# Performance work log

Hardware: AMD Instinct MI355X
Metric: run time of the kernel (lower is better)

The kernel has to match this reference:

```python
import jax, jax.numpy as jnp
import numpy as np

D_MODEL = 1024
HIDDEN = 64
N_STEPS = 6
T0, T1 = 0.0, 1.0


def setup_inputs() -> dict:
    key = jax.random.key(0)
    kx, k1, k2, k3, k4 = jax.random.split(key, 5)
    # PyTorch nn.Linear default init: U(-1/sqrt(fan_in), 1/sqrt(fan_in))
    s1 = 1.0 / np.sqrt(D_MODEL + 1)
    s2 = 1.0 / np.sqrt(HIDDEN)
    return {
        "x": jax.random.normal(kx, (8, 2048, D_MODEL), dtype=jnp.float32),
        "W1": jax.random.uniform(k1, (D_MODEL + 1, HIDDEN), jnp.float32, -s1, s1),
        "b1": jax.random.uniform(k2, (HIDDEN,), jnp.float32, -s1, s1),
        "W2": jax.random.uniform(k3, (HIDDEN, D_MODEL), jnp.float32, -s2, s2),
        "b2": jax.random.uniform(k4, (D_MODEL,), jnp.float32, -s2, s2),
    }


def _dynamics(t, z, W1, b1, W2, b2):
    # Equivalent to concat([z, t*ones], -1) @ W1: split the last row of W1
    # (the time channel) so we avoid materializing the concat.
    h = jnp.tanh(jnp.einsum("btd,dh->bth", z, W1[:-1]) + t * W1[-1] + b1)
    return jnp.einsum("bth,hd->btd", h, W2) + b2


def reference(x, W1, b1, W2, b2):
    h = (T1 - T0) / N_STEPS  # step size
    ts = T0 + h * jnp.arange(N_STEPS, dtype=x.dtype)

    def rk4_step(z, t):
        k1 = _dynamics(t, z, W1, b1, W2, b2)
        k2 = _dynamics(t + h / 2, z + (h / 2) * k1, W1, b1, W2, b2)
        k3 = _dynamics(t + h / 2, z + (h / 2) * k2, W1, b1, W2, b2)
        k4 = _dynamics(t + h, z + h * k3, W1, b1, W2, b2)
        z_next = z + (h / 6) * (k1 + 2 * k2 + 2 * k3 + k4)
        return z_next, None

    z_T, _ = jax.lax.scan(rk4_step, x, ts)
    return z_T
```

## Files before the change

### kernel.cpp

```cpp
#include <hip/hip_runtime.h>
#include <hip/hip_bf16.h>

#define DM 1024
#define HID 64
#define NSTEP 6
#define RSTEP (1.0f/6.0f)

using short8  = __attribute__((ext_vector_type(8))) short;
using short4v = __attribute__((ext_vector_type(4))) short;
using f32x4   = __attribute__((ext_vector_type(4))) float;

#define WS_W1P 0
#define WS_W2P 131072
#define WS_GP  262144
#define WS_U   270336
#define WS_VST 270592
#define WS_HU  276736

#define L_H   0
#define L_VST 2304
#define L_HU  8448
#define L_B2  8704
#define LDS_TOTAL 12800
#define HP 144

#define FENCE() asm volatile("s_waitcnt lgkmcnt(0)" ::: "memory")

__device__ __forceinline__ short f2bf(float f) {
    __hip_bfloat16 h = __float2bfloat16(f);
    short s;
    __builtin_memcpy(&s, &h, 2);
    return s;
}
__device__ __forceinline__ float ftanh(float x) {
    x = fminf(fmaxf(x, -10.f), 10.f);
    float e = __expf(2.f * x);
    return __fdividef(e - 1.f, e + 1.f);
}

__global__ void k_prep(const float* __restrict__ W1, const float* __restrict__ W2,
                       const float* __restrict__ b1, const float* __restrict__ b2,
                       short* __restrict__ W1P, short* __restrict__ W2P,
                       short* __restrict__ GP, float* __restrict__ U,
                       float* __restrict__ VST, float* __restrict__ HU) {
    __shared__ float red[4][64];
    int b = blockIdx.x;
    int t = threadIdx.x;
    int l = t & 63, q4 = t >> 6;
    if (b < 32) {
        int kk = b, c = q4;
        int col = c * 16 + (l & 15);
        int kb = kk * 32 + ((l >> 4) << 3);
        short8 v;
        #pragma unroll
        for (int i = 0; i < 8; ++i) v[i] = f2bf(W1[(kb + i) * HID + col]);
        *(short8*)(W1P + (((kk * 4 + c) * 64) + l) * 8) = v;
    } else if (b < 64) {
        int unit = (b - 32) * 4 + q4;
        int kk2 = unit >> 6, ct = unit & 63;
        int col = ct * 16 + (l & 15);
        int kb = kk2 * 32 + ((l >> 4) << 3);
        short8 v;
        #pragma unroll
        for (int i = 0; i < 8; ++i) v[i] = f2bf(W2[(kb + i) * DM + col]);
        *(short8*)(W2P + (((kk2 * 64 + ct) * 64) + l) * 8) = v;
    } else if (b < 128) {
        int j = b - 64;
        float acc = 0.f;
        #pragma unroll 8
        for (int d = q4 * 256; d < q4 * 256 + 256; ++d)
            acc += W2[j * DM + d] * W1[d * HID + l];
        red[q4][l] = acc;
        __syncthreads();
        if (t < 64) {
            float a = red[0][l] + red[1][l] + red[2][l] + red[3][l];
            int kk = j >> 5, lk = (j >> 3) & 3, ii = j & 7, c = l >> 4, lo = l & 15;
            GP[(((kk * 4 + c) * 64) + lk * 16 + lo) * 8 + ii] = f2bf(a);
        }
    } else {
        float acc = 0.f;
        #pragma unroll 8
        for (int d = q4 * 256; d < q4 * 256 + 256; ++d)
            acc += b2[d] * W1[d * HID + l];
        red[q4][l] = acc;
        __syncthreads();
        if (t < 64) {
            float uu = red[0][l] + red[1][l] + red[2][l] + red[3][l];
            U[l] = uu;
            HU[l] = RSTEP * uu;
            float b1l = b1[l];
            float wtl = W1[DM * HID + l];
            #pragma unroll
            for (int s6 = 0; s6 < 6; ++s6) {
                float ts = RSTEP * (float)s6;
                float tm = ts + 0.5f * RSTEP;
                float vmid = b1l + tm * wtl + 0.5f * RSTEP * uu;
                VST[(s6 * 4 + 0) * 64 + l] = b1l + ts * wtl;
                VST[(s6 * 4 + 1) * 64 + l] = vmid;
                VST[(s6 * 4 + 2) * 64 + l] = vmid;
                VST[(s6 * 4 + 3) * 64 + l] = b1l + (ts + RSTEP) * wtl + RSTEP * uu;
            }
        }
    }
}

#define EPL(W0,W1,W2,W3,X0,X1,P) \
    W0 = w2p8[(P) * 64 + lane];        W1 = w2p8[((P) + 64) * 64 + lane]; \
    W2 = w2p8[((P) + 1) * 64 + lane];  W3 = w2p8[((P) + 65) * 64 + lane]; \
    X0 = *(const f32x4*)(xrow + (P) * 16 + (hq << 2)); \
    X1 = *(const f32x4*)(xrow + ((P) + 1) * 16 + (hq << 2));

#define EPC(W0,W1,W2,W3,X0,X1,P) { \
    f32x4 p0 = (f32x4){0.f,0.f,0.f,0.f}, p1 = (f32x4){0.f,0.f,0.f,0.f}; \
    p0 = __builtin_amdgcn_mfma_f32_16x16x32_bf16(W0, sb0, p0, 0, 0, 0); \
    p0 = __builtin_amdgcn_mfma_f32_16x16x32_bf16(W1, sb1, p0, 0, 0, 0); \
    p1 = __builtin_amdgcn_mfma_f32_16x16x32_bf16(W2, sb0, p1, 0, 0, 0); \
    p1 = __builtin_amdgcn_mfma_f32_16x16x32_bf16(W3, sb1, p1, 0, 0, 0); \
    f32x4 b0v = *(const f32x4*)(smem + L_B2 + ((P) * 16 + (hq << 2)) * 4); \
    f32x4 b1v = *(const f32x4*)(smem + L_B2 + (((P) + 1) * 16 + (hq << 2)) * 4); \
    f32x4 n0, n1; \
    for (int j = 0; j < 4; ++j) { n0[j] = X0[j] + p0[j] + b0v[j]; \
                                  n1[j] = X1[j] + p1[j] + b1v[j]; } \
    *(f32x4*)(orow + (P) * 16 + (hq << 2)) = n0; \
    *(f32x4*)(orow + ((P) + 1) * 16 + (hq << 2)) = n1; }

__global__ __launch_bounds__(64) __attribute__((amdgpu_waves_per_eu(2, 4)))
void k_ode(
        const float* __restrict__ X, const float* __restrict__ b2,
        const short* __restrict__ W1P, const short* __restrict__ W2P,
        const short* __restrict__ GP, const float* __restrict__ VST,
        const float* __restrict__ HU, float* __restrict__ OUT) {
    extern __shared__ char smem[];
    const int lane = threadIdx.x & 63;
    const int hq = lane >> 4;
    const int l15 = lane & 15;
    const size_t row0 = (size_t)blockIdx.x * 16;
    const float* xrow = X + (row0 + l15) * DM;

    #pragma unroll
    for (int i = 0; i < 4; ++i)
        *(f32x4*)(smem + L_B2 + lane * 64 + i * 16) =
            *(const f32x4*)(b2 + lane * 16 + i * 4);

    f32x4 sz[4] = {(f32x4){0.f,0.f,0.f,0.f}, (f32x4){0.f,0.f,0.f,0.f},
                   (f32x4){0.f,0.f,0.f,0.f}, (f32x4){0.f,0.f,0.f,0.f}};
    {
        const short8* wp = (const short8*)W1P;
        #pragma unroll
        for (int B = 0; B < 4; ++B) {
            f32x4 lo[8], hi[8];
            #pragma unroll
            for (int i = 0; i < 8; ++i) {
                const float* xp = xrow + ((B * 8 + i) << 5) + (hq << 3);
                lo[i] = *(const f32x4*)(xp);
                hi[i] = *(const f32x4*)(xp + 4);
            }
            #pragma unroll
            for (int i = 0; i < 8; ++i) {
                int kk = B * 8 + i;
                short8 zf;
                #pragma unroll
                for (int j = 0; j < 4; ++j) { zf[j] = f2bf(lo[i][j]); zf[4 + j] = f2bf(hi[i][j]); }
                #pragma unroll
                for (int c = 0; c < 4; ++c)
                    sz[c] = __builtin_amdgcn_mfma_f32_16x16x32_bf16(
                                wp[(kk * 4 + c) * 64 + lane], zf, sz[c], 0, 0, 0);
            }
        }
    }

    #pragma unroll
    for (int i = 0; i < 6; ++i)
        *(f32x4*)(smem + L_VST + i * 1024 + lane * 16) =
            *(const f32x4*)(VST + i * 256 + lane * 4);
    if (lane < 16)
        *(f32x4*)(smem + L_HU + lane * 16) = *(const f32x4*)(HU + lane * 4);
    short8 gfr[2][4];
    #pragma unroll
    for (int k2 = 0; k2 < 2; ++k2)
        #pragma unroll
        for (int c = 0; c < 4; ++c)
            gfr[k2][c] = *(const short8*)(GP + ((k2 * 4 + c) * 64 + lane) * 8);
    FENCE();

    f32x4 ssum[4] = {(f32x4){0.f,0.f,0.f,0.f}, (f32x4){0.f,0.f,0.f,0.f},
                     (f32x4){0.f,0.f,0.f,0.f}, (f32x4){0.f,0.f,0.f,0.f}};

    for (int s = 0; s < NSTEP; ++s) {
        f32x4 hsum[4];

        #pragma unroll
        for (int c = 0; c < 4; ++c) {
            f32x4 vst = *(const f32x4*)(smem + L_VST + (s * 4 + 0) * 256 + c * 64 + (hq << 4));
            short4v hc;
            #pragma unroll
            for (int j = 0; j < 4; ++j) {
                float h = ftanh(sz[c][j] + vst[j]);
                hsum[c][j] = h;
                hc[j] = f2bf(h);
            }
            *(short4v*)(smem + L_H + l15 * HP + c * 32 + (hq << 3)) = hc;
        }
        FENCE();

        #pragma unroll
        for (int e = 1; e < 4; ++e) {
            const float ce = (e == 3) ? RSTEP : (0.5f * RSTEP);
            const float we = (e == 3) ? 1.f : 2.f;
            short8 hf0 = *(const short8*)(smem + L_H + l15 * HP + (hq << 4));
            short8 hf1 = *(const short8*)(smem + L_H + l15 * HP + 64 + (hq << 4));
            #pragma unroll
            for (int c = 0; c < 4; ++c) {
                f32x4 dd = (f32x4){0.f, 0.f, 0.f, 0.f};
                dd = __builtin_amdgcn_mfma_f32_16x16x32_bf16(gfr[0][c], hf0, dd, 0, 0, 0);
                dd = __builtin_amdgcn_mfma_f32_16x16x32_bf16(gfr[1][c], hf1, dd, 0, 0, 0);
                f32x4 vst = *(const f32x4*)(smem + L_VST + (s * 4 + e) * 256 + c * 64 + (hq << 4));
                short4v hc;
                #pragma unroll
                for (int j = 0; j < 4; ++j) {
                    float h = ftanh(sz[c][j] + ce * dd[j] + vst[j]);
                    hsum[c][j] += we * h;
                    if (e < 3) {
                        hc[j] = f2bf(h);
                    } else {
                        ssum[c][j] += hsum[c][j] * (RSTEP / 6.f);
                        hc[j] = (s < NSTEP - 1) ? f2bf(hsum[c][j] * (RSTEP / 6.f))
                                                : f2bf(ssum[c][j]);
                    }
                }
                *(short4v*)(smem + L_H + l15 * HP + c * 32 + (hq << 3)) = hc;
            }
            FENCE();
        }

        if (s < NSTEP - 1) {
            short8 hb0 = *(const short8*)(smem + L_H + l15 * HP + (hq << 4));
            short8 hb1 = *(const short8*)(smem + L_H + l15 * HP + 64 + (hq << 4));
            #pragma unroll
            for (int c = 0; c < 4; ++c) {
                f32x4 d = (f32x4){0.f, 0.f, 0.f, 0.f};
                d = __builtin_amdgcn_mfma_f32_16x16x32_bf16(gfr[0][c], hb0, d, 0, 0, 0);
                d = __builtin_amdgcn_mfma_f32_16x16x32_bf16(gfr[1][c], hb1, d, 0, 0, 0);
                f32x4 hu4 = *(const f32x4*)(smem + L_HU + c * 64 + (hq << 4));
                #pragma unroll
                for (int j = 0; j < 4; ++j)
                    sz[c][j] += d[j] + hu4[j];
            }
        }
    }

    {
        short8 sb0 = *(const short8*)(smem + L_H + l15 * HP + (hq << 4));
        short8 sb1 = *(const short8*)(smem + L_H + l15 * HP + 64 + (hq << 4));
        const short8* w2p8 = (const short8*)W2P;
        float* orow = OUT + (row0 + l15) * DM;

        short8 wA0, wA1, wA2, wA3; f32x4 xA0, xA1;
        short8 wB0, wB1, wB2, wB3; f32x4 xB0, xB1;
        EPL(wA0, wA1, wA2, wA3, xA0, xA1, 0)
        #pragma unroll
        for (int p = 0; p < 64; p += 4) {
            EPL(wB0, wB1, wB2, wB3, xB0, xB1, p + 2)
            EPC(wA0, wA1, wA2, wA3, xA0, xA1, p)
            if (p + 4 < 64) { EPL(wA0, wA1, wA2, wA3, xA0, xA1, p + 4) }
            EPC(wB0, wB1, wB2, wB3, xB0, xB1, p + 2)
        }
    }
}

extern "C" void kernel_launch(void* const* d_in, const int* in_sizes, int n_in,
                              void* d_out, int out_size, void* d_ws, size_t ws_size,
                              hipStream_t stream) {
    (void)in_sizes; (void)n_in; (void)out_size; (void)ws_size;
    const float* X  = (const float*)d_in[0];
    const float* W1 = (const float*)d_in[1];
    const float* b1 = (const float*)d_in[2];
    const float* W2 = (const float*)d_in[3];
    const float* b2 = (const float*)d_in[4];
    float* OUT = (float*)d_out;
    short* W1P = (short*)((char*)d_ws + WS_W1P);
    short* W2P = (short*)((char*)d_ws + WS_W2P);
    short* GP  = (short*)((char*)d_ws + WS_GP);
    float* U   = (float*)((char*)d_ws + WS_U);
    float* VST = (float*)((char*)d_ws + WS_VST);
    float* HU  = (float*)((char*)d_ws + WS_HU);

    k_prep<<<129, 256, 0, stream>>>(W1, W2, b1, b2, W1P, W2P, GP, U, VST, HU);
    k_ode<<<1024, 64, LDS_TOTAL, stream>>>(X, b2, W1P, W2P, GP, VST, HU, OUT);
}
```

Measured before the change: 72.14 us.

## Split hidden dimension across four waves per block with barrier-synchronized LDS exchange

```diff
diff --git a/kernel.cpp b/kernel.cpp
--- a/kernel.cpp
+++ b/kernel.cpp
@@ -17,14 +17,16 @@
 #define WS_VST 270592
 #define WS_HU  276736
 
-#define L_H   0
-#define L_VST 2304
-#define L_HU  8448
-#define L_B2  8704
-#define LDS_TOTAL 12800
+#define L_H0  0
+#define L_H1  2304
+#define L_HB  4608
+#define L_VST 6912
+#define L_HU  13056
+#define L_B2  13312
+#define LDS_TOTAL 17408
 #define HP 144
 
-#define FENCE() asm volatile("s_waitcnt lgkmcnt(0)" ::: "memory")
+#define BAR() asm volatile("s_waitcnt lgkmcnt(0)\n\ts_barrier" ::: "memory")
 
 __device__ __forceinline__ short f2bf(float f) {
     __hip_bfloat16 h = __float2bfloat16(f);
@@ -104,46 +106,53 @@
     }
 }
 
-#define EPL(W0,W1,W2,W3,X0,X1,P) \
-    W0 = w2p8[(P) * 64 + lane];        W1 = w2p8[((P) + 64) * 64 + lane]; \
-    W2 = w2p8[((P) + 1) * 64 + lane];  W3 = w2p8[((P) + 65) * 64 + lane]; \
-    X0 = *(const f32x4*)(xrow + (P) * 16 + (hq << 2)); \
-    X1 = *(const f32x4*)(xrow + ((P) + 1) * 16 + (hq << 2));
-
-#define EPC(W0,W1,W2,W3,X0,X1,P) { \
-    f32x4 p0 = (f32x4){0.f,0.f,0.f,0.f}, p1 = (f32x4){0.f,0.f,0.f,0.f}; \
-    p0 = __builtin_amdgcn_mfma_f32_16x16x32_bf16(W0, sb0, p0, 0, 0, 0); \
-    p0 = __builtin_amdgcn_mfma_f32_16x16x32_bf16(W1, sb1, p0, 0, 0, 0); \
-    p1 = __builtin_amdgcn_mfma_f32_16x16x32_bf16(W2, sb0, p1, 0, 0, 0); \
-    p1 = __builtin_amdgcn_mfma_f32_16x16x32_bf16(W3, sb1, p1, 0, 0, 0); \
-    f32x4 b0v = *(const f32x4*)(smem + L_B2 + ((P) * 16 + (hq << 2)) * 4); \
-    f32x4 b1v = *(const f32x4*)(smem + L_B2 + (((P) + 1) * 16 + (hq << 2)) * 4); \
-    f32x4 n0, n1; \
-    for (int j = 0; j < 4; ++j) { n0[j] = X0[j] + p0[j] + b0v[j]; \
-                                  n1[j] = X1[j] + p1[j] + b1v[j]; } \
-    *(f32x4*)(orow + (P) * 16 + (hq << 2)) = n0; \
-    *(f32x4*)(orow + ((P) + 1) * 16 + (hq << 2)) = n1; }
-
-__global__ __launch_bounds__(64) __attribute__((amdgpu_waves_per_eu(2, 4)))
+#define EPL(Wa,Wb,Wc,Wd,Xa,Xb,P) \
+    Wa = w2p8[(P) * 64 + lane];        Wb = w2p8[((P) + 64) * 64 + lane]; \
+    Wc = w2p8[((P) + 1) * 64 + lane];  Wd = w2p8[((P) + 65) * 64 + lane]; \
+    Xa = *(const f32x4*)(xrow + (P) * 16 + (hq << 2)); \
+    Xb = *(const f32x4*)(xrow + ((P) + 1) * 16 + (hq << 2));
+
+#define EPC(Wa,Wb,Wc,Wd,Xa,Xb,P) { \
+    f32x4 acc0 = (f32x4){0.f,0.f,0.f,0.f}, acc1 = (f32x4){0.f,0.f,0.f,0.f}; \
+    acc0 = __builtin_amdgcn_mfma_f32_16x16x32_bf16(Wa, sb0, acc0, 0, 0, 0); \
+    acc0 = __builtin_amdgcn_mfma_f32_16x16x32_bf16(Wb, sb1, acc0, 0, 0, 0); \
+    acc1 = __builtin_amdgcn_mfma_f32_16x16x32_bf16(Wc, sb0, acc1, 0, 0, 0); \
+    acc1 = __builtin_amdgcn_mfma_f32_16x16x32_bf16(Wd, sb1, acc1, 0, 0, 0); \
+    f32x4 epc_bv0 = *(const f32x4*)(smem + L_B2 + ((P) * 16 + (hq << 2)) * 4); \
+    f32x4 epc_bv1 = *(const f32x4*)(smem + L_B2 + (((P) + 1) * 16 + (hq << 2)) * 4); \
+    f32x4 epc_n0, epc_n1; \
+    for (int j = 0; j < 4; ++j) { epc_n0[j] = Xa[j] + acc0[j] + epc_bv0[j]; \
+                                  epc_n1[j] = Xb[j] + acc1[j] + epc_bv1[j]; } \
+    *(f32x4*)(orow + (P) * 16 + (hq << 2)) = epc_n0; \
+    *(f32x4*)(orow + ((P) + 1) * 16 + (hq << 2)) = epc_n1; }
+
+__global__ __launch_bounds__(256) __attribute__((amdgpu_waves_per_eu(2, 4)))
 void k_ode(
         const float* __restrict__ X, const float* __restrict__ b2,
         const short* __restrict__ W1P, const short* __restrict__ W2P,
         const short* __restrict__ GP, const float* __restrict__ VST,
         const float* __restrict__ HU, float* __restrict__ OUT) {
     extern __shared__ char smem[];
-    const int lane = threadIdx.x & 63;
+    const int t = threadIdx.x;
+    const int lane = t & 63;
+    const int w = t >> 6;
     const int hq = lane >> 4;
     const int l15 = lane & 15;
+    const int hcol0 = w * 16 + hq * 4;
     const size_t row0 = (size_t)blockIdx.x * 16;
     const float* xrow = X + (row0 + l15) * DM;
 
-    #pragma unroll
-    for (int i = 0; i < 4; ++i)
-        *(f32x4*)(smem + L_B2 + lane * 64 + i * 16) =
-            *(const f32x4*)(b2 + lane * 16 + i * 4);
-
-    f32x4 sz[4] = {(f32x4){0.f,0.f,0.f,0.f}, (f32x4){0.f,0.f,0.f,0.f},
-                   (f32x4){0.f,0.f,0.f,0.f}, (f32x4){0.f,0.f,0.f,0.f}};
+    *(f32x4*)(smem + L_B2 + t * 16) = *(const f32x4*)(b2 + t * 4);
+    *(f32x4*)(smem + L_VST + t * 16) = *(const f32x4*)(VST + t * 4);
+    if (t < 128)
+        *(f32x4*)(smem + L_VST + 4096 + t * 16) = *(const f32x4*)(VST + 1024 + t * 4);
+    else if (t < 144)
+        *(f32x4*)(smem + L_HU + (t - 128) * 16) = *(const f32x4*)(HU + (t - 128) * 4);
+
+    short8 gf0 = *(const short8*)(GP + (w * 64 + lane) * 8);
+    short8 gf1 = *(const short8*)(GP + ((4 + w) * 64 + lane) * 8);
+
+    f32x4 sz = (f32x4){0.f, 0.f, 0.f, 0.f};
     {
         const short8* wp = (const short8*)W1P;
         #pragma unroll
@@ -161,109 +170,90 @@
                 short8 zf;
                 #pragma unroll
                 for (int j = 0; j < 4; ++j) { zf[j] = f2bf(lo[i][j]); zf[4 + j] = f2bf(hi[i][j]); }
-                #pragma unroll
-                for (int c = 0; c < 4; ++c)
-                    sz[c] = __builtin_amdgcn_mfma_f32_16x16x32_bf16(
-                                wp[(kk * 4 + c) * 64 + lane], zf, sz[c], 0, 0, 0);
-            }
-        }
-    }
-
-    #pragma unroll
-    for (int i = 0; i < 6; ++i)
-        *(f32x4*)(smem + L_VST + i * 1024 + lane * 16) =
-            *(const f32x4*)(VST + i * 256 + lane * 4);
-    if (lane < 16)
-        *(f32x4*)(smem + L_HU + lane * 16) = *(const f32x4*)(HU + lane * 4);
-    short8 gfr[2][4];
-    #pragma unroll
-    for (int k2 = 0; k2 < 2; ++k2)
-        #pragma unroll
-        for (int c = 0; c < 4; ++c)
-            gfr[k2][c] = *(const short8*)(GP + ((k2 * 4 + c) * 64 + lane) * 8);
-    FENCE();
-
-    f32x4 ssum[4] = {(f32x4){0.f,0.f,0.f,0.f}, (f32x4){0.f,0.f,0.f,0.f},
-                     (f32x4){0.f,0.f,0.f,0.f}, (f32x4){0.f,0.f,0.f,0.f}};
+                sz = __builtin_amdgcn_mfma_f32_16x16x32_bf16(
+                         wp[(kk * 4 + w) * 64 + lane], zf, sz, 0, 0, 0);
+            }
+        }
+    }
+    BAR();
+
+    f32x4 ssum = (f32x4){0.f, 0.f, 0.f, 0.f};
 
     for (int s = 0; s < NSTEP; ++s) {
-        f32x4 hsum[4];
-
-        #pragma unroll
-        for (int c = 0; c < 4; ++c) {
-            f32x4 vst = *(const f32x4*)(smem + L_VST + (s * 4 + 0) * 256 + c * 64 + (hq << 4));
+        f32x4 hsum;
+
+        {
+            f32x4 vst = *(const f32x4*)(smem + L_VST + (s * 4 + 0) * 256 + hcol0 * 4);
             short4v hc;
             #pragma unroll
             for (int j = 0; j < 4; ++j) {
-                float h = ftanh(sz[c][j] + vst[j]);
-                hsum[c][j] = h;
+                float h = ftanh(sz[j] + vst[j]);
+                hsum[j] = h;
                 hc[j] = f2bf(h);
             }
-            *(short4v*)(smem + L_H + l15 * HP + c * 32 + (hq << 3)) = hc;
-        }
-        FENCE();
+            *(short4v*)(smem + L_H0 + l15 * HP + hcol0 * 2) = hc;
+        }
+        BAR();
 
         #pragma unroll
         for (int e = 1; e < 4; ++e) {
             const float ce = (e == 3) ? RSTEP : (0.5f * RSTEP);
             const float we = (e == 3) ? 1.f : 2.f;
-            short8 hf0 = *(const short8*)(smem + L_H + l15 * HP + (hq << 4));
-            short8 hf1 = *(const short8*)(smem + L_H + l15 * HP + 64 + (hq << 4));
-            #pragma unroll
-            for (int c = 0; c < 4; ++c) {
-                f32x4 dd = (f32x4){0.f, 0.f, 0.f, 0.f};
-                dd = __builtin_amdgcn_mfma_f32_16x16x32_bf16(gfr[0][c], hf0, dd, 0, 0, 0);
-                dd = __builtin_amdgcn_mfma_f32_16x16x32_bf16(gfr[1][c], hf1, dd, 0, 0, 0);
-                f32x4 vst = *(const f32x4*)(smem + L_VST + (s * 4 + e) * 256 + c * 64 + (hq << 4));
-                short4v hc;
-                #pragma unroll
-                for (int j = 0; j < 4; ++j) {
-                    float h = ftanh(sz[c][j] + ce * dd[j] + vst[j]);
-                    hsum[c][j] += we * h;
-                    if (e < 3) {
-                        hc[j] = f2bf(h);
-                    } else {
-                        ssum[c][j] += hsum[c][j] * (RSTEP / 6.f);
-                        hc[j] = (s < NSTEP - 1) ? f2bf(hsum[c][j] * (RSTEP / 6.f))
-                                                : f2bf(ssum[c][j]);
-                    }
+            const int rbuf = (e == 2) ? L_H1 : L_H0;
+            const int wbuf = (e == 1) ? L_H1 : ((e == 2) ? L_H0 : L_HB);
+
+            short8 hf0 = *(const short8*)(smem + rbuf + l15 * HP + (hq << 4));
+            short8 hf1 = *(const short8*)(smem + rbuf + l15 * HP + 64 + (hq << 4));
+            f32x4 dd = (f32x4){0.f, 0.f, 0.f, 0.f};
+            dd = __builtin_amdgcn_mfma_f32_16x16x32_bf16(gf0, hf0, dd, 0, 0, 0);
+            dd = __builtin_amdgcn_mfma_f32_16x16x32_bf16(gf1, hf1, dd, 0, 0, 0);
+            f32x4 vst = *(const f32x4*)(smem + L_VST + (s * 4 + e) * 256 + hcol0 * 4);
+            short4v hc;
+            #pragma unroll
+            for (int j = 0; j < 4; ++j) {
+                float h = ftanh(sz[j] + ce * dd[j] + vst[j]);
+                hsum[j] += we * h;
+                if (e < 3) {
+                    hc[j] = f2bf(h);
+                } else {
+                    ssum[j] += hsum[j] * (RSTEP / 6.f);
+                    hc[j] = (s < NSTEP - 1) ? f2bf(hsum[j] * (RSTEP / 6.f))
+                                            : f2bf(ssum[j]);
                 }
-                *(short4v*)(smem + L_H + l15 * HP + c * 32 + (hq << 3)) = hc;
-            }
-            FENCE();
+            }
+            *(short4v*)(smem + wbuf + l15 * HP + hcol0 * 2) = hc;
+            BAR();
         }
 
         if (s < NSTEP - 1) {
-            short8 hb0 = *(const short8*)(smem + L_H + l15 * HP + (hq << 4));
-            short8 hb1 = *(const short8*)(smem + L_H + l15 * HP + 64 + (hq << 4));
-            #pragma unroll
-            for (int c = 0; c < 4; ++c) {
-                f32x4 d = (f32x4){0.f, 0.f, 0.f, 0.f};
-                d = __builtin_amdgcn_mfma_f32_16x16x32_bf16(gfr[0][c], hb0, d, 0, 0, 0);
-                d = __builtin_amdgcn_mfma_f32_16x16x32_bf16(gfr[1][c], hb1, d, 0, 0, 0);
-                f32x4 hu4 = *(const f32x4*)(smem + L_HU + c * 64 + (hq << 4));
-                #pragma unroll
-                for (int j = 0; j < 4; ++j)
-                    sz[c][j] += d[j] + hu4[j];
-            }
+            short8 hb0 = *(const short8*)(smem + L_HB + l15 * HP + (hq << 4));
+            short8 hb1 = *(const short8*)(smem + L_HB + l15 * HP + 64 + (hq << 4));
+            f32x4 d = (f32x4){0.f, 0.f, 0.f, 0.f};
+            d = __builtin_amdgcn_mfma_f32_16x16x32_bf16(gf0, hb0, d, 0, 0, 0);
+            d = __builtin_amdgcn_mfma_f32_16x16x32_bf16(gf1, hb1, d, 0, 0, 0);
+            f32x4 hu4 = *(const f32x4*)(smem + L_HU + hcol0 * 4);
+            #pragma unroll
+            for (int j = 0; j < 4; ++j)
+                sz[j] += d[j] + hu4[j];
         }
     }
 
     {
-        short8 sb0 = *(const short8*)(smem + L_H + l15 * HP + (hq << 4));
-        short8 sb1 = *(const short8*)(smem + L_H + l15 * HP + 64 + (hq << 4));
+        short8 sb0 = *(const short8*)(smem + L_HB + l15 * HP + (hq << 4));
+        short8 sb1 = *(const short8*)(smem + L_HB + l15 * HP + 64 + (hq << 4));
         const short8* w2p8 = (const short8*)W2P;
         float* orow = OUT + (row0 + l15) * DM;
+        const int ctbase = w * 16;
 
         short8 wA0, wA1, wA2, wA3; f32x4 xA0, xA1;
         short8 wB0, wB1, wB2, wB3; f32x4 xB0, xB1;
-        EPL(wA0, wA1, wA2, wA3, xA0, xA1, 0)
-        #pragma unroll
-        for (int p = 0; p < 64; p += 4) {
-            EPL(wB0, wB1, wB2, wB3, xB0, xB1, p + 2)
-            EPC(wA0, wA1, wA2, wA3, xA0, xA1, p)
-            if (p + 4 < 64) { EPL(wA0, wA1, wA2, wA3, xA0, xA1, p + 4) }
-            EPC(wB0, wB1, wB2, wB3, xB0, xB1, p + 2)
+        EPL(wA0, wA1, wA2, wA3, xA0, xA1, ctbase)
+        #pragma unroll
+        for (int p = 0; p < 16; p += 4) {
+            EPL(wB0, wB1, wB2, wB3, xB0, xB1, ctbase + p + 2)
+            EPC(wA0, wA1, wA2, wA3, xA0, xA1, ctbase + p)
+            if (p + 4 < 16) { EPL(wA0, wA1, wA2, wA3, xA0, xA1, ctbase + p + 4) }
+            EPC(wB0, wB1, wB2, wB3, xB0, xB1, ctbase + p + 2)
         }
     }
 }
@@ -286,5 +276,5 @@
     float* HU  = (float*)((char*)d_ws + WS_HU);
 
     k_prep<<<129, 256, 0, stream>>>(W1, W2, b1, b2, W1P, W2P, GP, U, VST, HU);
-    k_ode<<<1024, 64, LDS_TOTAL, stream>>>(X, b2, W1P, W2P, GP, VST, HU, OUT);
-}
+    k_ode<<<1024, 256, LDS_TOTAL, stream>>>(X, b2, W1P, W2P, GP, VST, HU, OUT);
+}
```

After: 77.45 us. 7.4% more time.
